# Performance work log

Hardware: AMD Instinct MI355X
Metric: run time of the kernel (lower is better)

The kernel has to match this reference:

```python
import jax, jax.numpy as jnp
import numpy as np

IN_F, OUT_F = 128, 128
R, LEV, N = 2, 2, 8192
JD = (R - 1) * LEV + 1  # 3 filter levels


def setup_inputs() -> dict:
    key = jax.random.key(0)
    ks = jax.random.split(key, 7)
    x = jax.random.normal(ks[0], (N, IN_F), dtype=jnp.float32)
    d_list = jax.random.uniform(ks[1], (JD, N), dtype=jnp.float32)
    U = jax.random.normal(ks[2], (N, N), dtype=jnp.float32)
    Vt = jax.random.normal(ks[3], (N, N), dtype=jnp.float32)
    # learned params
    bound = float(np.sqrt(6.0 / (IN_F + OUT_F)))  # xavier_uniform
    weight = jax.random.uniform(ks[4], (IN_F, OUT_F), dtype=jnp.float32, minval=-bound, maxval=bound)
    filt = jax.random.uniform(ks[5], (JD, N), dtype=jnp.float32, minval=0.9, maxval=1.1)
    bias = jnp.zeros((OUT_F,), dtype=jnp.float32)
    return {"x": x, "d_list": d_list, "U": U, "Vt": Vt, "weight": weight, "filt": filt, "bias": bias}


def reference(x, d_list, U, Vt, weight, filt, bias):
    # Original loop: sum_j U @ ((d_j * f_j * d_j)[:, None] * (Vt @ (x @ W)))
    # By linearity this equals U @ ((sum_j d_j^2 * f_j)[:, None] * (Vt @ (x @ W)))
    # -- same math, with Vt@xw computed once and U applied once.
    xw = x @ weight                                  # [N, out]
    Vxw = Vt @ xw                                    # [N, out]
    scale = jnp.sum(d_list * filt * d_list, axis=0)  # [N]
    out = U @ (scale[:, None] * Vxw)                 # [N, out]
    return out + bias
```

## Files before the change

kernel.cpp:

```cpp
#include <hip/hip_runtime.h>

typedef short s8v __attribute__((ext_vector_type(8)));
typedef float f32x4 __attribute__((ext_vector_type(4)));

#define BM 32
#define KC 64
#define PAD 72

__device__ __forceinline__ unsigned short f2bf(float x) {
    unsigned int u = __float_as_uint(x);
    u += 0x7fffu + ((u >> 16) & 1u);
    return (unsigned short)(u >> 16);
}

__global__ __launch_bounds__(256, 2) void gemm_kernel(
    const float* __restrict__ A, int lda,
    const unsigned short* __restrict__ Bt, int ldb,
    float* __restrict__ C, int klen)
{
    __shared__ __align__(16) unsigned short As[2][BM * PAD];
    __shared__ __align__(16) unsigned short Bs[2][128 * PAD];

    const int t    = threadIdx.x;
    const int wave = t >> 6;
    const int lane = t & 63;
    const int quad = lane >> 4;
    const int l16  = lane & 15;

    const int mbase = blockIdx.x * BM;
    const int k0    = blockIdx.y * klen;
    C += (size_t)blockIdx.y * gridDim.x * BM * 128;

    const int ar  = t >> 3;
    const int akg = (t & 7) * 8;
    const float*          Ap = A  + (size_t)(mbase + ar) * lda + k0 + akg;
    const unsigned short* Bp = Bt + (size_t)ar * ldb + k0 + akg;

    const int nchunks = klen / KC;

    {
        float4 a0 = *(const float4*)(Ap);
        float4 a1 = *(const float4*)(Ap + 4);
        s8v b0 = *(const s8v*)(Bp);
        s8v b1 = *(const s8v*)(Bp + (size_t)32 * ldb);
        s8v b2 = *(const s8v*)(Bp + (size_t)64 * ldb);
        s8v b3 = *(const s8v*)(Bp + (size_t)96 * ldb);
        s8v av;
        av[0] = (short)f2bf(a0.x); av[1] = (short)f2bf(a0.y);
        av[2] = (short)f2bf(a0.z); av[3] = (short)f2bf(a0.w);
        av[4] = (short)f2bf(a1.x); av[5] = (short)f2bf(a1.y);
        av[6] = (short)f2bf(a1.z); av[7] = (short)f2bf(a1.w);
        *(s8v*)&As[0][ar * PAD + akg] = av;
        *(s8v*)&Bs[0][(ar +  0) * PAD + akg] = b0;
        *(s8v*)&Bs[0][(ar + 32) * PAD + akg] = b1;
        *(s8v*)&Bs[0][(ar + 64) * PAD + akg] = b2;
        *(s8v*)&Bs[0][(ar + 96) * PAD + akg] = b3;
    }
    __syncthreads();

    f32x4 acc00 = {0.f,0.f,0.f,0.f}, acc01 = {0.f,0.f,0.f,0.f};
    f32x4 acc10 = {0.f,0.f,0.f,0.f}, acc11 = {0.f,0.f,0.f,0.f};

    const int arow0 = l16 * PAD;
    const int arow1 = (16 + l16) * PAD;
    const int brow0 = (wave * 32 + l16) * PAD;
    const int brow1 = (wave * 32 + 16 + l16) * PAD;
    const int kq    = quad * 8;

    for (int c = 0; c < nchunks; ++c) {
        const int  cur = c & 1;
        const bool pf  = (c + 1 < nchunks);
        float4 a0, a1; s8v b0, b1, b2, b3;
        if (pf) {
            const size_t o = (size_t)(c + 1) * KC;
            a0 = *(const float4*)(Ap + o);
            a1 = *(const float4*)(Ap + o + 4);
            b0 = *(const s8v*)(Bp + o);
            b1 = *(const s8v*)(Bp + o + (size_t)32 * ldb);
            b2 = *(const s8v*)(Bp + o + (size_t)64 * ldb);
            b3 = *(const s8v*)(Bp + o + (size_t)96 * ldb);
        }
        const unsigned short* as = As[cur];
        const unsigned short* bs = Bs[cur];
        #pragma unroll
        for (int kk = 0; kk < 2; ++kk) {
            const int ko = kk * 32 + kq;
            s8v af0 = *(const s8v*)&as[arow0 + ko];
            s8v af1 = *(const s8v*)&as[arow1 + ko];
            s8v bg0 = *(const s8v*)&bs[brow0 + ko];
            s8v bg1 = *(const s8v*)&bs[brow1 + ko];
            acc00 = __builtin_amdgcn_mfma_f32_16x16x32_bf16(af0, bg0, acc00, 0, 0, 0);
            acc01 = __builtin_amdgcn_mfma_f32_16x16x32_bf16(af0, bg1, acc01, 0, 0, 0);
            acc10 = __builtin_amdgcn_mfma_f32_16x16x32_bf16(af1, bg0, acc10, 0, 0, 0);
            acc11 = __builtin_amdgcn_mfma_f32_16x16x32_bf16(af1, bg1, acc11, 0, 0, 0);
        }
        if (pf) {
            const int nb = cur ^ 1;
            s8v av;
            av[0] = (short)f2bf(a0.x); av[1] = (short)f2bf(a0.y);
            av[2] = (short)f2bf(a0.z); av[3] = (short)f2bf(a0.w);
            av[4] = (short)f2bf(a1.x); av[5] = (short)f2bf(a1.y);
            av[6] = (short)f2bf(a1.z); av[7] = (short)f2bf(a1.w);
            *(s8v*)&As[nb][ar * PAD + akg] = av;
            *(s8v*)&Bs[nb][(ar +  0) * PAD + akg] = b0;
            *(s8v*)&Bs[nb][(ar + 32) * PAD + akg] = b1;
            *(s8v*)&Bs[nb][(ar + 64) * PAD + akg] = b2;
            *(s8v*)&Bs[nb][(ar + 96) * PAD + akg] = b3;
        }
        __syncthreads();
    }

    const int col = wave * 32 + l16;
    const int row = mbase + quad * 4;
    #pragma unroll
    for (int i = 0; i < 4; ++i) {
        C[(size_t)(row + i)      * 128 + col]      = acc00[i];
        C[(size_t)(row + i)      * 128 + col + 16] = acc01[i];
        C[(size_t)(row + 16 + i) * 128 + col]      = acc10[i];
        C[(size_t)(row + 16 + i) * 128 + col + 16] = acc11[i];
    }
}

__global__ __launch_bounds__(256) void tkern(
    const float* __restrict__ a, const float* __restrict__ b,
    const float* __restrict__ dl, const float* __restrict__ ft,
    unsigned short* __restrict__ out, int nrows, int mode)
{
    __shared__ __align__(16) unsigned short L[128 * PAD];
    const int t    = threadIdx.x;
    const int kb   = blockIdx.x * 64;
    const int kloc = t >> 2;
    const int fseg = (t & 3) * 32;
    const int k    = kb + kloc;

    float s = 1.0f;
    if (mode) {
        float s0 = 0.f;
        #pragma unroll
        for (int j = 0; j < 3; ++j) {
            float d = dl[(size_t)j * nrows + k];
            s0 += d * d * ft[(size_t)j * nrows + k];
        }
        s = s0;
    }
    const float* ap = a + (size_t)k * 128 + fseg;
    const float* bp = b + (size_t)k * 128 + fseg;
    #pragma unroll
    for (int i = 0; i < 8; ++i) {
        float4 v = *(const float4*)(ap + i * 4);
        if (mode) {
            float4 w = *(const float4*)(bp + i * 4);
            v.x += w.x; v.y += w.y; v.z += w.z; v.w += w.w;
        }
        const int fb = fseg + i * 4;
        L[(fb + 0) * PAD + kloc] = f2bf(v.x * s);
        L[(fb + 1) * PAD + kloc] = f2bf(v.y * s);
        L[(fb + 2) * PAD + kloc] = f2bf(v.z * s);
        L[(fb + 3) * PAD + kloc] = f2bf(v.w * s);
    }
    __syncthreads();
    const int f    = t >> 1;
    const int half = (t & 1) * 32;
    unsigned short* op = out + (size_t)f * nrows + kb + half;
    #pragma unroll
    for (int i = 0; i < 4; ++i) {
        *(s8v*)(op + i * 8) = *(const s8v*)&L[f * PAD + half + i * 8];
    }
}

__global__ __launch_bounds__(256) void addbias_kernel(
    const float* __restrict__ p0, const float* __restrict__ p1,
    const float* __restrict__ bias, float* __restrict__ out)
{
    const size_t e = ((size_t)blockIdx.x * 256 + threadIdx.x) * 4;
    float4 x = *(const float4*)(p0 + e);
    float4 y = *(const float4*)(p1 + e);
    float4 bb = *(const float4*)(bias + (e & 127));
    float4 r;
    r.x = x.x + y.x + bb.x;
    r.y = x.y + y.y + bb.y;
    r.z = x.z + y.z + bb.z;
    r.w = x.w + y.w + bb.w;
    *(float4*)(out + e) = r;
}

extern "C" void kernel_launch(void* const* d_in, const int* in_sizes, int n_in,
                              void* d_out, int out_size, void* d_ws, size_t ws_size,
                              hipStream_t stream)
{
    const float* x  = (const float*)d_in[0];
    const float* dl = (const float*)d_in[1];
    const float* U  = (const float*)d_in[2];
    const float* Vt = (const float*)d_in[3];
    const float* W  = (const float*)d_in[4];
    const float* ft = (const float*)d_in[5];
    const float* bs = (const float*)d_in[6];
    float* out = (float*)d_out;

    const int N = 8192, F = 128;
    char* ws = (char*)d_ws;
    unsigned short* Wt  = (unsigned short*)(ws);
    unsigned short* xwt = (unsigned short*)(ws + (64 << 10));
    unsigned short* yt  = (unsigned short*)(ws + (64 << 10) + (2 << 20));
    float* bufA = (float*)(ws + (64 << 10) + (4 << 20));
    float* bufB = (float*)(ws + (64 << 10) + (12 << 20));

    tkern<<<dim3(F / 64), 256, 0, stream>>>(W, nullptr, nullptr, nullptr, Wt, F, 0);
    gemm_kernel<<<dim3(N / BM, 1), 256, 0, stream>>>(x, F, Wt, F, bufA, F);
    tkern<<<dim3(N / 64), 256, 0, stream>>>(bufA, nullptr, nullptr, nullptr, xwt, N, 0);
    gemm_kernel<<<dim3(N / BM, 2), 256, 0, stream>>>(Vt, N, xwt, N, bufB, N / 2);
    tkern<<<dim3(N / 64), 256, 0, stream>>>(bufB, bufB + (size_t)N * F, dl, ft, yt, N, 1);
    gemm_kernel<<<dim3(N / BM, 2), 256, 0, stream>>>(U, N, yt, N, bufA, N / 2);
    addbias_kernel<<<dim3((N * F) / (256 * 4)), 256, 0, stream>>>(
        bufA, bufA + (size_t)N * F, bs, out);
}
```

Before: 598.3 us.

## Enlarge GEMM M-tile, prefetch two chunks ahead, and use 4-way split-K

The GEMM tile height doubles to 64 rows, so each B fragment is reused across four row tiles. Global loads are now issued two K-chunks ahead through register double buffering, and the barrier waits only on LDS traffic, not on global loads. Split-K rises from 2 to 4 to keep the block count unchanged, and the reduction kernels now sum four partial slabs. This costs more registers and more partial-sum traffic in exchange for deeper latency hiding on the streamed U and Vt reads.

```diff
diff --git a/kernel.cpp b/kernel.cpp
--- a/kernel.cpp
+++ b/kernel.cpp
@@ -3,9 +3,11 @@
 typedef short s8v __attribute__((ext_vector_type(8)));
 typedef float f32x4 __attribute__((ext_vector_type(4)));
 
-#define BM 32
+#define BM 64
 #define KC 64
 #define PAD 72
+
+#define LDS_BARRIER() asm volatile("s_waitcnt lgkmcnt(0)\n\ts_barrier" ::: "memory")
 
 __device__ __forceinline__ unsigned short f2bf(float x) {
     unsigned int u = __float_as_uint(x);
@@ -22,107 +24,137 @@
     __shared__ __align__(16) unsigned short Bs[2][128 * PAD];
 
     const int t    = threadIdx.x;
-    const int wave = t >> 6;
+    const int w    = t >> 6;
     const int lane = t & 63;
     const int quad = lane >> 4;
     const int l16  = lane & 15;
+    const int w32  = w * 32;
+    const int kq   = quad * 8;
 
     const int mbase = blockIdx.x * BM;
     const int k0    = blockIdx.y * klen;
     C += (size_t)blockIdx.y * gridDim.x * BM * 128;
 
-    const int ar  = t >> 3;
-    const int akg = (t & 7) * 8;
-    const float*          Ap = A  + (size_t)(mbase + ar) * lda + k0 + akg;
-    const unsigned short* Bp = Bt + (size_t)ar * ldb + k0 + akg;
+    const int ar = t >> 2;
+    const int ak = (t & 3) * 16;
+    const int br = t >> 1;
+    const int bk = (t & 1) * 32;
+    const float*          Ap = A  + (size_t)(mbase + ar) * lda + k0 + ak;
+    const unsigned short* Bp = Bt + (size_t)br * ldb + k0 + bk;
 
     const int nchunks = klen / KC;
 
+    float4 a_r[2][4];
+    s8v    b_r[2][4];
+
     {
-        float4 a0 = *(const float4*)(Ap);
-        float4 a1 = *(const float4*)(Ap + 4);
-        s8v b0 = *(const s8v*)(Bp);
-        s8v b1 = *(const s8v*)(Bp + (size_t)32 * ldb);
-        s8v b2 = *(const s8v*)(Bp + (size_t)64 * ldb);
-        s8v b3 = *(const s8v*)(Bp + (size_t)96 * ldb);
-        s8v av;
-        av[0] = (short)f2bf(a0.x); av[1] = (short)f2bf(a0.y);
-        av[2] = (short)f2bf(a0.z); av[3] = (short)f2bf(a0.w);
-        av[4] = (short)f2bf(a1.x); av[5] = (short)f2bf(a1.y);
-        av[6] = (short)f2bf(a1.z); av[7] = (short)f2bf(a1.w);
-        *(s8v*)&As[0][ar * PAD + akg] = av;
-        *(s8v*)&Bs[0][(ar +  0) * PAD + akg] = b0;
-        *(s8v*)&Bs[0][(ar + 32) * PAD + akg] = b1;
-        *(s8v*)&Bs[0][(ar + 64) * PAD + akg] = b2;
-        *(s8v*)&Bs[0][(ar + 96) * PAD + akg] = b3;
-    }
-    __syncthreads();
-
-    f32x4 acc00 = {0.f,0.f,0.f,0.f}, acc01 = {0.f,0.f,0.f,0.f};
-    f32x4 acc10 = {0.f,0.f,0.f,0.f}, acc11 = {0.f,0.f,0.f,0.f};
-
-    const int arow0 = l16 * PAD;
-    const int arow1 = (16 + l16) * PAD;
-    const int brow0 = (wave * 32 + l16) * PAD;
-    const int brow1 = (wave * 32 + 16 + l16) * PAD;
-    const int kq    = quad * 8;
-
-    for (int c = 0; c < nchunks; ++c) {
-        const int  cur = c & 1;
-        const bool pf  = (c + 1 < nchunks);
-        float4 a0, a1; s8v b0, b1, b2, b3;
-        if (pf) {
-            const size_t o = (size_t)(c + 1) * KC;
-            a0 = *(const float4*)(Ap + o);
-            a1 = *(const float4*)(Ap + o + 4);
-            b0 = *(const s8v*)(Bp + o);
-            b1 = *(const s8v*)(Bp + o + (size_t)32 * ldb);
-            b2 = *(const s8v*)(Bp + o + (size_t)64 * ldb);
-            b3 = *(const s8v*)(Bp + o + (size_t)96 * ldb);
-        }
-        const unsigned short* as = As[cur];
-        const unsigned short* bs = Bs[cur];
-        #pragma unroll
-        for (int kk = 0; kk < 2; ++kk) {
-            const int ko = kk * 32 + kq;
-            s8v af0 = *(const s8v*)&as[arow0 + ko];
-            s8v af1 = *(const s8v*)&as[arow1 + ko];
-            s8v bg0 = *(const s8v*)&bs[brow0 + ko];
-            s8v bg1 = *(const s8v*)&bs[brow1 + ko];
-            acc00 = __builtin_amdgcn_mfma_f32_16x16x32_bf16(af0, bg0, acc00, 0, 0, 0);
-            acc01 = __builtin_amdgcn_mfma_f32_16x16x32_bf16(af0, bg1, acc01, 0, 0, 0);
-            acc10 = __builtin_amdgcn_mfma_f32_16x16x32_bf16(af1, bg0, acc10, 0, 0, 0);
-            acc11 = __builtin_amdgcn_mfma_f32_16x16x32_bf16(af1, bg1, acc11, 0, 0, 0);
-        }
-        if (pf) {
-            const int nb = cur ^ 1;
-            s8v av;
-            av[0] = (short)f2bf(a0.x); av[1] = (short)f2bf(a0.y);
-            av[2] = (short)f2bf(a0.z); av[3] = (short)f2bf(a0.w);
-            av[4] = (short)f2bf(a1.x); av[5] = (short)f2bf(a1.y);
-            av[6] = (short)f2bf(a1.z); av[7] = (short)f2bf(a1.w);
-            *(s8v*)&As[nb][ar * PAD + akg] = av;
-            *(s8v*)&Bs[nb][(ar +  0) * PAD + akg] = b0;
-            *(s8v*)&Bs[nb][(ar + 32) * PAD + akg] = b1;
-            *(s8v*)&Bs[nb][(ar + 64) * PAD + akg] = b2;
-            *(s8v*)&Bs[nb][(ar + 96) * PAD + akg] = b3;
-        }
-        __syncthreads();
-    }
-
-    const int col = wave * 32 + l16;
-    const int row = mbase + quad * 4;
-    #pragma unroll
-    for (int i = 0; i < 4; ++i) {
-        C[(size_t)(row + i)      * 128 + col]      = acc00[i];
-        C[(size_t)(row + i)      * 128 + col + 16] = acc01[i];
-        C[(size_t)(row + 16 + i) * 128 + col]      = acc10[i];
-        C[(size_t)(row + 16 + i) * 128 + col + 16] = acc11[i];
+        #pragma unroll
+        for (int i = 0; i < 4; ++i) a_r[0][i] = *(const float4*)(Ap + i * 4);
+        #pragma unroll
+        for (int i = 0; i < 4; ++i) b_r[0][i] = *(const s8v*)(Bp + i * 8);
+        s8v v0, v1;
+        v0[0] = (short)f2bf(a_r[0][0].x); v0[1] = (short)f2bf(a_r[0][0].y);
+        v0[2] = (short)f2bf(a_r[0][0].z); v0[3] = (short)f2bf(a_r[0][0].w);
+        v0[4] = (short)f2bf(a_r[0][1].x); v0[5] = (short)f2bf(a_r[0][1].y);
+        v0[6] = (short)f2bf(a_r[0][1].z); v0[7] = (short)f2bf(a_r[0][1].w);
+        v1[0] = (short)f2bf(a_r[0][2].x); v1[1] = (short)f2bf(a_r[0][2].y);
+        v1[2] = (short)f2bf(a_r[0][2].z); v1[3] = (short)f2bf(a_r[0][2].w);
+        v1[4] = (short)f2bf(a_r[0][3].x); v1[5] = (short)f2bf(a_r[0][3].y);
+        v1[6] = (short)f2bf(a_r[0][3].z); v1[7] = (short)f2bf(a_r[0][3].w);
+        *(s8v*)&As[0][ar * PAD + ak]     = v0;
+        *(s8v*)&As[0][ar * PAD + ak + 8] = v1;
+        #pragma unroll
+        for (int i = 0; i < 4; ++i) *(s8v*)&Bs[0][br * PAD + bk + 8 * i] = b_r[0][i];
+        if (nchunks > 1) {
+            #pragma unroll
+            for (int i = 0; i < 4; ++i) a_r[1][i] = *(const float4*)(Ap + KC + i * 4);
+            #pragma unroll
+            for (int i = 0; i < 4; ++i) b_r[1][i] = *(const s8v*)(Bp + KC + i * 8);
+        }
+    }
+    LDS_BARRIER();
+
+    f32x4 acc[4][2];
+    #pragma unroll
+    for (int rt = 0; rt < 4; ++rt)
+        #pragma unroll
+        for (int ct = 0; ct < 2; ++ct)
+            acc[rt][ct] = (f32x4){0.f, 0.f, 0.f, 0.f};
+
+#define GITER(p)                                                               \
+    {                                                                          \
+        if (c + 2 < nchunks) {                     \
+            const size_t o = (size_t)(c + 2) * KC;                             \
+            _Pragma("unroll")                                                  \
+            for (int i = 0; i < 4; ++i) a_r[p][i] = *(const float4*)(Ap + o + i * 4); \
+            _Pragma("unroll")                                                  \
+            for (int i = 0; i < 4; ++i) b_r[p][i] = *(const s8v*)(Bp + o + i * 8);    \
+        }                                                                      \
+        {                                                \
+            const unsigned short* as = As[p];                                  \
+            const unsigned short* bs = Bs[p];                                  \
+            _Pragma("unroll")                                                  \
+            for (int kk = 0; kk < 2; ++kk) {                                   \
+                const int ko = kk * 32 + kq;                                   \
+                s8v af[4], bf[2];                                              \
+                _Pragma("unroll")                                              \
+                for (int rt = 0; rt < 4; ++rt)                                 \
+                    af[rt] = *(const s8v*)&as[(rt * 16 + l16) * PAD + ko];     \
+                _Pragma("unroll")                                              \
+                for (int ct = 0; ct < 2; ++ct)                                 \
+                    bf[ct] = *(const s8v*)&bs[(w32 + ct * 16 + l16) * PAD + ko]; \
+                _Pragma("unroll")                                              \
+                for (int rt = 0; rt < 4; ++rt)                                 \
+                    _Pragma("unroll")                                          \
+                    for (int ct = 0; ct < 2; ++ct)                             \
+                        acc[rt][ct] = __builtin_amdgcn_mfma_f32_16x16x32_bf16( \
+                            af[rt], bf[ct], acc[rt][ct], 0, 0, 0);             \
+            }                                                                  \
+        }                                                                      \
+        if (c + 1 < nchunks) {   \
+            const int q = (p) ^ 1;                                             \
+            s8v v0, v1;                                                        \
+            v0[0] = (short)f2bf(a_r[q][0].x); v0[1] = (short)f2bf(a_r[q][0].y);\
+            v0[2] = (short)f2bf(a_r[q][0].z); v0[3] = (short)f2bf(a_r[q][0].w);\
+            v0[4] = (short)f2bf(a_r[q][1].x); v0[5] = (short)f2bf(a_r[q][1].y);\
+            v0[6] = (short)f2bf(a_r[q][1].z); v0[7] = (short)f2bf(a_r[q][1].w);\
+            v1[0] = (short)f2bf(a_r[q][2].x); v1[1] = (short)f2bf(a_r[q][2].y);\
+            v1[2] = (short)f2bf(a_r[q][2].z); v1[3] = (short)f2bf(a_r[q][2].w);\
+            v1[4] = (short)f2bf(a_r[q][3].x); v1[5] = (short)f2bf(a_r[q][3].y);\
+            v1[6] = (short)f2bf(a_r[q][3].z); v1[7] = (short)f2bf(a_r[q][3].w);\
+            *(s8v*)&As[q][ar * PAD + ak]     = v0;                             \
+            *(s8v*)&As[q][ar * PAD + ak + 8] = v1;                             \
+            _Pragma("unroll")                                                  \
+            for (int i = 0; i < 4; ++i)                                        \
+                *(s8v*)&Bs[q][br * PAD + bk + 8 * i] = b_r[q][i];              \
+        }                                                                      \
+        LDS_BARRIER();                                                         \
+    }
+
+    int c = 0;
+    while (true) {
+        GITER(0)
+        if (++c == nchunks) break;
+        GITER(1)
+        if (++c == nchunks) break;
+    }
+#undef GITER
+
+    #pragma unroll
+    for (int rt = 0; rt < 4; ++rt) {
+        const int row = mbase + rt * 16 + quad * 4;
+        #pragma unroll
+        for (int ct = 0; ct < 2; ++ct) {
+            const int col = w32 + ct * 16 + l16;
+            #pragma unroll
+            for (int i = 0; i < 4; ++i)
+                C[(size_t)(row + i) * 128 + col] = acc[rt][ct][i];
+        }
     }
 }
 
 __global__ __launch_bounds__(256) void tkern(
-    const float* __restrict__ a, const float* __restrict__ b,
+    const float* __restrict__ a, int nslabs,
     const float* __restrict__ dl, const float* __restrict__ ft,
     unsigned short* __restrict__ out, int nrows, int mode)
 {
@@ -132,6 +164,7 @@
     const int kloc = t >> 2;
     const int fseg = (t & 3) * 32;
     const int k    = kb + kloc;
+    const size_t slab = (size_t)nrows * 128;
 
     float s = 1.0f;
     if (mode) {
@@ -144,13 +177,12 @@
         s = s0;
     }
     const float* ap = a + (size_t)k * 128 + fseg;
-    const float* bp = b + (size_t)k * 128 + fseg;
     #pragma unroll
     for (int i = 0; i < 8; ++i) {
         float4 v = *(const float4*)(ap + i * 4);
-        if (mode) {
-            float4 w = *(const float4*)(bp + i * 4);
-            v.x += w.x; v.y += w.y; v.z += w.z; v.w += w.w;
+        for (int sl = 1; sl < nslabs; ++sl) {
+            float4 u = *(const float4*)(ap + sl * slab + i * 4);
+            v.x += u.x; v.y += u.y; v.z += u.z; v.w += u.w;
         }
         const int fb = fseg + i * 4;
         L[(fb + 0) * PAD + kloc] = f2bf(v.x * s);
@@ -169,18 +201,17 @@
 }
 
 __global__ __launch_bounds__(256) void addbias_kernel(
-    const float* __restrict__ p0, const float* __restrict__ p1,
-    const float* __restrict__ bias, float* __restrict__ out)
+    const float* __restrict__ p, const float* __restrict__ bias,
+    float* __restrict__ out)
 {
     const size_t e = ((size_t)blockIdx.x * 256 + threadIdx.x) * 4;
-    float4 x = *(const float4*)(p0 + e);
-    float4 y = *(const float4*)(p1 + e);
-    float4 bb = *(const float4*)(bias + (e & 127));
-    float4 r;
-    r.x = x.x + y.x + bb.x;
-    r.y = x.y + y.y + bb.y;
-    r.z = x.z + y.z + bb.z;
-    r.w = x.w + y.w + bb.w;
+    const size_t slab = (size_t)8192 * 128;
+    float4 r = *(const float4*)(bias + (e & 127));
+    #pragma unroll
+    for (int s = 0; s < 4; ++s) {
+        float4 x = *(const float4*)(p + s * slab + e);
+        r.x += x.x; r.y += x.y; r.z += x.z; r.w += x.w;
+    }
     *(float4*)(out + e) = r;
 }
 
@@ -198,19 +229,19 @@
     float* out = (float*)d_out;
 
     const int N = 8192, F = 128;
+    const int SPLITK = 4;
     char* ws = (char*)d_ws;
     unsigned short* Wt  = (unsigned short*)(ws);
     unsigned short* xwt = (unsigned short*)(ws + (64 << 10));
     unsigned short* yt  = (unsigned short*)(ws + (64 << 10) + (2 << 20));
     float* bufA = (float*)(ws + (64 << 10) + (4 << 20));
-    float* bufB = (float*)(ws + (64 << 10) + (12 << 20));
-
-    tkern<<<dim3(F / 64), 256, 0, stream>>>(W, nullptr, nullptr, nullptr, Wt, F, 0);
+    float* bufB = (float*)(ws + (64 << 10) + (20 << 20));
+
+    tkern<<<dim3(F / 64), 256, 0, stream>>>(W, 1, nullptr, nullptr, Wt, F, 0);
     gemm_kernel<<<dim3(N / BM, 1), 256, 0, stream>>>(x, F, Wt, F, bufA, F);
-    tkern<<<dim3(N / 64), 256, 0, stream>>>(bufA, nullptr, nullptr, nullptr, xwt, N, 0);
-    gemm_kernel<<<dim3(N / BM, 2), 256, 0, stream>>>(Vt, N, xwt, N, bufB, N / 2);
-    tkern<<<dim3(N / 64), 256, 0, stream>>>(bufB, bufB + (size_t)N * F, dl, ft, yt, N, 1);
-    gemm_kernel<<<dim3(N / BM, 2), 256, 0, stream>>>(U, N, yt, N, bufA, N / 2);
-    addbias_kernel<<<dim3((N * F) / (256 * 4)), 256, 0, stream>>>(
-        bufA, bufA + (size_t)N * F, bs, out);
-}
+    tkern<<<dim3(N / 64), 256, 0, stream>>>(bufA, 1, nullptr, nullptr, xwt, N, 0);
+    gemm_kernel<<<dim3(N / BM, SPLITK), 256, 0, stream>>>(Vt, N, xwt, N, bufB, N / SPLITK);
+    tkern<<<dim3(N / 64), 256, 0, stream>>>(bufB, SPLITK, dl, ft, yt, N, 1);
+    gemm_kernel<<<dim3(N / BM, SPLITK), 256, 0, stream>>>(U, N, yt, N, bufA, N / SPLITK);
+    addbias_kernel<<<dim3((N * F) / (256 * 4)), 256, 0, stream>>>(bufA, bs, out);
+}
```

New measurement: 611.9 us. 2.3% more time.
